# Kernel optimization log

Hardware: AMD Instinct MI355X
Metric: run time of the kernel (lower is better)

The kernel has to match this reference:

```python
import jax, jax.numpy as jnp
import numpy as np

B, N, K, C_IN, C_OUT = 4, 8192, 32, 64, 64
MID = (C_OUT + C_IN) // 2  # 64, since C_IN is even
GROUPS = 8
EPS = 1e-5
SLOPE = 0.1


def group_norm(x, gamma, beta, groups=GROUPS, eps=EPS):
    # x: [b, ..., C], normalize per-sample over all spatial dims and group channels
    b = x.shape[0]
    C = x.shape[-1]
    xr = x.reshape(b, -1, groups, C // groups)
    mean = xr.mean(axis=(1, 3), keepdims=True)
    var = xr.var(axis=(1, 3), keepdims=True)
    xn = ((xr - mean) / jnp.sqrt(var + eps)).reshape(x.shape)
    return xn * gamma + beta


def lrelu(x):
    return jnp.where(x >= 0, x, SLOPE * x)


def setup_inputs() -> dict:
    key = jax.random.key(0)
    ks = jax.random.split(key, 10)
    signal = jax.random.normal(ks[0], (B, N, C_IN), dtype=jnp.float32)
    edges = jax.random.randint(ks[1], (B * N * K,), 0, B * N, dtype=jnp.int64)
    edge_feats = jax.random.normal(ks[2], (B * N * K, 3), dtype=jnp.float32)
    W1 = jax.random.normal(ks[3], (MID, C_IN + 3), dtype=jnp.float32) * 0.1
    W2 = jax.random.normal(ks[4], (C_OUT, MID), dtype=jnp.float32) * 0.1
    W3 = jax.random.normal(ks[5], (C_OUT, C_OUT), dtype=jnp.float32) * 0.1
    return {
        "signal": signal, "edges": edges, "edge_feats": edge_feats,
        "W1": W1, "g1": jnp.ones((MID,), jnp.float32), "b1": jnp.zeros((MID,), jnp.float32),
        "W2": W2, "g2": jnp.ones((C_OUT,), jnp.float32), "b2": jnp.zeros((C_OUT,), jnp.float32),
        "W3": W3, "g3": jnp.ones((C_OUT,), jnp.float32), "b3": jnp.zeros((C_OUT,), jnp.float32),
    }


def reference(signal, edges, edge_feats, W1, g1, b1, W2, g2, b2, W3, g3, b3):
    b, n, c = signal.shape
    k = edges.shape[0] // (b * n)
    flat = signal.reshape(b * n, c)
    # gather neighbor features and take relative difference: [b*n, k, c]
    ef = flat[edges].reshape(b * n, k, c) - flat[:, None, :]
    # concat relative coordinates -> [b, n, k, c+3]
    x = jnp.concatenate([ef, edge_feats.reshape(b * n, k, 3)], axis=-1)
    x = x.reshape(b, n, k, c + 3)
    # 1x1 conv (fc1) + GN + lrelu
    x = jnp.einsum('bnkc,mc->bnkm', x, W1)
    x = lrelu(group_norm(x, g1, b1))
    # max-pool over neighbors -> [b, n, mid]
    x = jnp.max(x, axis=2)
    # fc2 + GN + lrelu
    x = jnp.einsum('bnm,om->bno', x, W2)
    x = lrelu(group_norm(x, g2, b2))
    # fc3 + GN + lrelu
    x = jnp.einsum('bno,po->bnp', x, W3)
    x = lrelu(group_norm(x, g3, b3))
    return x  # [b, n, nb_feat_out]
```

## Files before the change

### kernel.cpp

```cpp
#include <hip/hip_runtime.h>

#define NB    4
#define NPB   8192
#define NPTS  (NB*NPB)
#define KNB   32
#define CH    64
#define W1C   67
#define EPSV  1e-5f
#define SLOPEV 0.1f

typedef float f32x2 __attribute__((ext_vector_type(2)));
typedef float f32x4 __attribute__((ext_vector_type(4)));
typedef short bf16x8 __attribute__((ext_vector_type(8)));
typedef unsigned short u16;
typedef u16 u16x4 __attribute__((ext_vector_type(4)));
typedef u16 u16x8 __attribute__((ext_vector_type(8)));

#define WS_STATS1 0
#define WS_STATS2 64
#define WS_STATS3 128
#define WS_YB     256
#define WS_MX     (WS_YB + NPTS*CH/2)
#define WS_MN     (WS_MX + NPTS*CH/2)

#define LDPW 68
#define SEDS (KNB*4 + 4)
#define EPB  64

__device__ __forceinline__ u16 f2bf(float f) {
    unsigned u = __float_as_uint(f);
    u += 0x7fff + ((u >> 16) & 1);
    return (u16)(u >> 16);
}
__device__ __forceinline__ float bf2f(u16 h) {
    return __uint_as_float(((unsigned)h) << 16);
}

__device__ __forceinline__ bool probe_is32(const int* e_i32, int tid) {
    int found = 0;
    #pragma unroll
    for (int i = 0; i < 8; ++i)
        found |= (e_i32[(tid*8 + i)*2 + 1] != 0);
    return (__ballot(found) != 0ull);
}

template<int MODE>
__global__ __launch_bounds__(256) void k_mm(
    const void* __restrict__ X0, const void* __restrict__ X1,
    const float* __restrict__ Wg,
    const float* __restrict__ statsIn, float invcnt,
    const float* __restrict__ gm, const float* __restrict__ bt,
    u16* __restrict__ Out, float* __restrict__ statsOut,
    float* __restrict__ zeroStats)
{
    __shared__ u16 Wl[64*LDPW];
    __shared__ __align__(16) float affA[64];
    __shared__ __align__(16) float affB[64];
    __shared__ float lacc[16];
    int tid = threadIdx.x;
    int pbase = blockIdx.x * 64;
    int b = pbase >> 13;

    if (MODE == 0 && blockIdx.x == 0 && tid < 192) zeroStats[tid] = 0.f;
    if (MODE != 0) {
        if (tid < 64) {
            int g = tid >> 3;
            float sv = statsIn[b*16 + g*2 + 0];
            float qv = statsIn[b*16 + g*2 + 1];
            float mean = sv * invcnt;
            float var  = fmaf(-mean, mean, qv * invcnt);
            float rstd = rsqrtf(var + EPSV);
            float a = gm[tid] * rstd;
            affA[tid] = a;
            affB[tid] = fmaf(-mean, a, bt[tid]);
        }
        if (tid < 16) lacc[tid] = 0.f;
    }
    {
        const int wstride = (MODE == 0) ? W1C : 64;
        #pragma unroll
        for (int i = 0; i < 16; ++i) {
            int e = tid + 256*i;
            int o = e >> 6, m = e & 63;
            Wl[o*LDPW + m] = f2bf(Wg[o*wstride + m]);
        }
    }
    __syncthreads();

    int l = tid & 63, w = tid >> 6;
    int lr = l & 15, lk = l >> 4;
    int row = pbase + w*16 + lr;

    bf16x8 af[2];
    #pragma unroll
    for (int kh = 0; kh < 2; ++kh) {
        int m0 = kh*32 + lk*8;
        bf16x8 h;
        if (MODE == 0) {
            f32x4 a0 = *(const f32x4*)&((const float*)X0)[row*64 + m0];
            f32x4 a1 = *(const f32x4*)&((const float*)X0)[row*64 + m0 + 4];
            #pragma unroll
            for (int j = 0; j < 4; ++j) {
                h[j]   = (short)f2bf(a0[j]);
                h[4+j] = (short)f2bf(a1[j]);
            }
        } else {
            float aA[8], aB[8];
            *(f32x4*)&aA[0] = *(const f32x4*)&affA[m0];
            *(f32x4*)&aA[4] = *(const f32x4*)&affA[m0+4];
            *(f32x4*)&aB[0] = *(const f32x4*)&affB[m0];
            *(f32x4*)&aB[4] = *(const f32x4*)&affB[m0+4];
            u16x8 vx = *(const u16x8*)&((const u16*)X0)[row*64 + m0];
            if (MODE == 1) {
                u16x8 vn = *(const u16x8*)&((const u16*)X1)[row*64 + m0];
                #pragma unroll
                for (int j = 0; j < 8; ++j) {
                    float a = aA[j];
                    float x = (a < 0.f) ? bf2f(vn[j]) : bf2f(vx[j]);
                    float z = fmaf(a, x, aB[j]);
                    z = (z >= 0.f) ? z : SLOPEV * z;
                    h[j] = (short)f2bf(z);
                }
            } else {
                #pragma unroll
                for (int j = 0; j < 8; ++j) {
                    float z = fmaf(aA[j], bf2f(vx[j]), aB[j]);
                    z = (z >= 0.f) ? z : SLOPEV * z;
                    h[j] = (short)f2bf(z);
                }
            }
        }
        af[kh] = h;
    }

    bf16x8 bw[4][2];
    #pragma unroll
    for (int ot = 0; ot < 4; ++ot)
        #pragma unroll
        for (int kh = 0; kh < 2; ++kh)
            bw[ot][kh] = *(const bf16x8*)&Wl[(ot*16 + lr)*LDPW + kh*32 + lk*8];

    f32x4 acc[4];
    #pragma unroll
    for (int ot = 0; ot < 4; ++ot) {
        f32x4 c = {0.f, 0.f, 0.f, 0.f};
        c = __builtin_amdgcn_mfma_f32_16x16x32_bf16(af[0], bw[ot][0], c, 0, 0, 0);
        c = __builtin_amdgcn_mfma_f32_16x16x32_bf16(af[1], bw[ot][1], c, 0, 0, 0);
        acc[ot] = c;
    }

    #pragma unroll
    for (int ot = 0; ot < 4; ++ot)
        #pragma unroll
        for (int r = 0; r < 4; ++r) {
            int p = pbase + w*16 + lk*4 + r;
            int o = ot*16 + lr;
            Out[p*64 + o] = f2bf(acc[ot][r]);
        }

    if (MODE != 0) {
        #pragma unroll
        for (int ot = 0; ot < 4; ++ot) {
            float s = 0.f, ss = 0.f;
            #pragma unroll
            for (int r = 0; r < 4; ++r) {
                float v = acc[ot][r];
                s += v;
                ss = fmaf(v, v, ss);
            }
            s += __shfl_xor(s, 16, 64);  ss += __shfl_xor(ss, 16, 64);
            s += __shfl_xor(s, 32, 64);  ss += __shfl_xor(ss, 32, 64);
            s += __shfl_xor(s, 1, 64);   ss += __shfl_xor(ss, 1, 64);
            s += __shfl_xor(s, 2, 64);   ss += __shfl_xor(ss, 2, 64);
            s += __shfl_xor(s, 4, 64);   ss += __shfl_xor(ss, 4, 64);
            if ((l & 7) == 0 && l < 16) {
                int g = ot*2 + (l >> 3);
                atomicAdd(&lacc[g*2 + 0], s);
                atomicAdd(&lacc[g*2 + 1], ss);
            }
        }
        __syncthreads();
        if (tid < 16)
            atomicAdd(&statsOut[b*16 + tid], lacc[tid]);
    }
}

__global__ __launch_bounds__(512) void k_edge(
    const u16* __restrict__ Yb, const void* __restrict__ edg,
    const float* __restrict__ ef, const float* __restrict__ W1,
    u16* __restrict__ Mx, u16* __restrict__ Mn, float* __restrict__ stats1)
{
    __shared__ float sed[EPB*SEDS];
    __shared__ float lacc[16];
    int tid = threadIdx.x;
    if (tid < 16) lacc[tid] = 0.f;

    bool is32 = probe_is32((const int*)edg, tid);
    {
        const int* e32 = (const int*)edg;
        const long long* e64 = (const long long*)edg;
        int ebase = blockIdx.x * (EPB*KNB);
        #pragma unroll
        for (int i = 0; i < 4; ++i) {
            int idx = tid + i*512;
            int gi  = ebase + idx;
            int e   = is32 ? __builtin_nontemporal_load(e32 + gi)
                           : (int)__builtin_nontemporal_load(e64 + gi);
            int pt = idx >> 5, k = idx & 31;
            float* d = &sed[pt*SEDS + k*4];
            d[0] = __builtin_nontemporal_load(ef + gi*3 + 0);
            d[1] = __builtin_nontemporal_load(ef + gi*3 + 1);
            d[2] = __builtin_nontemporal_load(ef + gi*3 + 2);
            d[3] = __int_as_float(e << 7);
        }
    }

    int lane = tid & 63, wv = tid >> 6;
    int il = lane & 7;
    int g8 = lane >> 3;
    int lpt = wv*8 + g8;
    int p = blockIdx.x * EPB + lpt;

    f32x2 w0[4], w1[4], w2[4];
    #pragma unroll
    for (int jj = 0; jj < 4; ++jj) {
        int ch = il*8 + jj*2;
        w0[jj] = (f32x2){W1[ch*W1C + 64], W1[(ch+1)*W1C + 64]};
        w1[jj] = (f32x2){W1[ch*W1C + 65], W1[(ch+1)*W1C + 65]};
        w2[jj] = (f32x2){W1[ch*W1C + 66], W1[(ch+1)*W1C + 66]};
    }
    f32x2 yp[4], mx[4], mn[4];
    u16x8 yh = *(const u16x8*)&Yb[p*64 + il*8];
    #pragma unroll
    for (int jj = 0; jj < 4; ++jj) {
        yp[jj] = (f32x2){bf2f(yh[jj*2]), bf2f(yh[jj*2+1])};
        mx[jj] = (f32x2){-3.4e38f, -3.4e38f};
        mn[jj] = (f32x2){ 3.4e38f,  3.4e38f};
    }
    f32x2 s2 = {0.f, 0.f}, ss2 = {0.f, 0.f};
    __syncthreads();

    const char* Ybase = (const char*)Yb + il*16;
    const float* sp = &sed[lpt*SEDS];
    #pragma unroll 8
    for (int k = 0; k < KNB; ++k) {
        f32x4 m4 = *(const f32x4*)(sp + k*4);
        u16x8 q = *(const u16x8*)(Ybase + __float_as_int(m4[3]));
        f32x2 c0v = m4[0], c1v = m4[1], c2v = m4[2];
        #pragma unroll
        for (int jj = 0; jj < 4; ++jj) {
            f32x2 qq = {bf2f(q[jj*2]), bf2f(q[jj*2+1])};
            f32x2 t = qq - yp[jj];
            t = __builtin_elementwise_fma(c0v, w0[jj], t);
            t = __builtin_elementwise_fma(c1v, w1[jj], t);
            t = __builtin_elementwise_fma(c2v, w2[jj], t);
            mx[jj] = __builtin_elementwise_max(mx[jj], t);
            mn[jj] = __builtin_elementwise_min(mn[jj], t);
            s2 += t;
            ss2 = __builtin_elementwise_fma(t, t, ss2);
        }
    }

    u16x8 hx, hn;
    #pragma unroll
    for (int jj = 0; jj < 4; ++jj) {
        hx[jj*2] = f2bf(mx[jj].x); hx[jj*2+1] = f2bf(mx[jj].y);
        hn[jj*2] = f2bf(mn[jj].x); hn[jj*2+1] = f2bf(mn[jj].y);
    }
    __builtin_nontemporal_store(hx, (u16x8*)(Mx + p*64 + il*8));
    __builtin_nontemporal_store(hn, (u16x8*)(Mn + p*64 + il*8));

    float s  = s2.x + s2.y;
    float ss = ss2.x + ss2.y;
    s += __shfl_xor(s,  8, 64);  ss += __shfl_xor(ss,  8, 64);
    s += __shfl_xor(s, 16, 64);  ss += __shfl_xor(ss, 16, 64);
    s += __shfl_xor(s, 32, 64);  ss += __shfl_xor(ss, 32, 64);
    if (lane < 8) {
        atomicAdd(&lacc[lane*2 + 0], s);
        atomicAdd(&lacc[lane*2 + 1], ss);
    }
    __syncthreads();
    if (tid < 16) {
        int b = (blockIdx.x * EPB) >> 13;
        atomicAdd(&stats1[b*16 + tid], lacc[tid]);
    }
}

__global__ __launch_bounds__(256) void k_out(
    const u16* __restrict__ z3, const float* __restrict__ stats,
    const float* __restrict__ g3, const float* __restrict__ b3,
    float* __restrict__ out)
{
    const float invcnt = 1.f/(float)(NPB*8);
    int tid = threadIdx.x;
    int pbase = blockIdx.x * 64;
    int b = pbase >> 13;
    #pragma unroll
    for (int it = 0; it < 4; ++it) {
        int flat = it*1024 + tid*4;
        int p = pbase + (flat >> 6);
        int m = flat & 63;
        int g = m >> 3;
        float sv = stats[b*16 + g*2 + 0];
        float qv = stats[b*16 + g*2 + 1];
        float mean = sv * invcnt;
        float var  = fmaf(-mean, mean, qv * invcnt);
        float rstd = rsqrtf(var + EPSV);
        u16x4 v = *(const u16x4*)&z3[p*64 + m];
        float r[4];
        #pragma unroll
        for (int j = 0; j < 4; ++j) {
            float aa = g3[m+j] * rstd;
            float z  = fmaf(aa, bf2f(v[j]) - mean, b3[m+j]);
            r[j] = (z >= 0.f) ? z : SLOPEV * z;
        }
        f32x4 o4 = {r[0], r[1], r[2], r[3]};
        *(f32x4*)&out[p*64 + m] = o4;
    }
}

extern "C" void kernel_launch(void* const* d_in, const int* in_sizes, int n_in,
                              void* d_out, int out_size, void* d_ws, size_t ws_size,
                              hipStream_t stream)
{
    const float* sig = (const float*)d_in[0];
    const void*  edg = d_in[1];
    const float* ef  = (const float*)d_in[2];
    const float* W1  = (const float*)d_in[3];
    const float* g1  = (const float*)d_in[4];
    const float* b1  = (const float*)d_in[5];
    const float* W2  = (const float*)d_in[6];
    const float* g2  = (const float*)d_in[7];
    const float* b2  = (const float*)d_in[8];
    const float* W3  = (const float*)d_in[9];
    const float* g3  = (const float*)d_in[10];
    const float* b3  = (const float*)d_in[11];
    float* out = (float*)d_out;
    float* ws  = (float*)d_ws;
    u16*   yb  = (u16*)(ws + WS_YB);
    u16*   mxb = (u16*)(ws + WS_MX);
    u16*   mnb = (u16*)(ws + WS_MN);

    k_mm<0><<<NPTS/64, 256, 0, stream>>>(sig, nullptr, W1, nullptr, 0.f,
                                         nullptr, nullptr, yb, nullptr, ws);
    k_edge<<<NPTS/EPB, 512, 0, stream>>>(yb, edg, ef, W1, mxb, mnb,
                                         ws + WS_STATS1);
    k_mm<1><<<NPTS/64, 256, 0, stream>>>(mxb, mnb, W2, ws + WS_STATS1,
                                         1.f/(float)(NPB*KNB*8), g1, b1,
                                         yb, ws + WS_STATS2, nullptr);
    k_mm<2><<<NPTS/64, 256, 0, stream>>>(yb, nullptr, W3, ws + WS_STATS2,
                                         1.f/(float)(NPB*8), g2, b2,
                                         mxb, ws + WS_STATS3, nullptr);
    k_out<<<NPTS/64, 256, 0, stream>>>(mxb, ws + WS_STATS3, g3, b3, out);
}
```

Measured before the change: 57.42 us.

## Fuse edge, fc2, fc3 and output stages into persistent kernel with grid barriers

```diff
diff --git a/kernel.cpp b/kernel.cpp
--- a/kernel.cpp
+++ b/kernel.cpp
@@ -8,24 +8,24 @@
 #define W1C   67
 #define EPSV  1e-5f
 #define SLOPEV 0.1f
+#define MBLK  256
+#define MPPB  128
 
 typedef float f32x2 __attribute__((ext_vector_type(2)));
 typedef float f32x4 __attribute__((ext_vector_type(4)));
 typedef short bf16x8 __attribute__((ext_vector_type(8)));
 typedef unsigned short u16;
-typedef u16 u16x4 __attribute__((ext_vector_type(4)));
 typedef u16 u16x8 __attribute__((ext_vector_type(8)));
 
-#define WS_STATS1 0
-#define WS_STATS2 64
-#define WS_STATS3 128
-#define WS_YB     256
-#define WS_MX     (WS_YB + NPTS*CH/2)
-#define WS_MN     (WS_MX + NPTS*CH/2)
-
-#define LDPW 68
-#define SEDS (KNB*4 + 4)
-#define EPB  64
+#define WS_STATS 0
+#define WS_CTR   192
+#define WS_YB    256
+#define WS_PK    (WS_YB + NPTS*CH/2)
+
+#define LDW 68
+
+#define INV1 (1.f/(float)(NPB*KNB*8))
+#define INV2 (1.f/(float)(NPB*8))
 
 __device__ __forceinline__ u16 f2bf(float f) {
     unsigned u = __float_as_uint(f);
@@ -35,7 +35,6 @@
 __device__ __forceinline__ float bf2f(u16 h) {
     return __uint_as_float(((unsigned)h) << 16);
 }
-
 __device__ __forceinline__ bool probe_is32(const int* e_i32, int tid) {
     int found = 0;
     #pragma unroll
@@ -44,278 +43,365 @@
     return (__ballot(found) != 0ull);
 }
 
-template<int MODE>
-__global__ __launch_bounds__(256) void k_mm(
-    const void* __restrict__ X0, const void* __restrict__ X1,
-    const float* __restrict__ Wg,
-    const float* __restrict__ statsIn, float invcnt,
-    const float* __restrict__ gm, const float* __restrict__ bt,
-    u16* __restrict__ Out, float* __restrict__ statsOut,
-    float* __restrict__ zeroStats)
+__global__ __launch_bounds__(256) void k_pre(
+    const float* __restrict__ sig, const void* __restrict__ edg,
+    const float* __restrict__ ef, const float* __restrict__ W1,
+    u16* __restrict__ Yb, float* __restrict__ pk, float* __restrict__ ws)
 {
-    __shared__ u16 Wl[64*LDPW];
-    __shared__ __align__(16) float affA[64];
-    __shared__ __align__(16) float affB[64];
-    __shared__ float lacc[16];
+    __shared__ u16 Wl[64*LDW];
     int tid = threadIdx.x;
-    int pbase = blockIdx.x * 64;
-    int b = pbase >> 13;
-
-    if (MODE == 0 && blockIdx.x == 0 && tid < 192) zeroStats[tid] = 0.f;
-    if (MODE != 0) {
-        if (tid < 64) {
-            int g = tid >> 3;
-            float sv = statsIn[b*16 + g*2 + 0];
-            float qv = statsIn[b*16 + g*2 + 1];
-            float mean = sv * invcnt;
-            float var  = fmaf(-mean, mean, qv * invcnt);
-            float rstd = rsqrtf(var + EPSV);
-            float a = gm[tid] * rstd;
-            affA[tid] = a;
-            affB[tid] = fmaf(-mean, a, bt[tid]);
-        }
-        if (tid < 16) lacc[tid] = 0.f;
-    }
-    {
-        const int wstride = (MODE == 0) ? W1C : 64;
-        #pragma unroll
-        for (int i = 0; i < 16; ++i) {
-            int e = tid + 256*i;
-            int o = e >> 6, m = e & 63;
-            Wl[o*LDPW + m] = f2bf(Wg[o*wstride + m]);
-        }
+    int blk = blockIdx.x;
+
+    if (blk >= 512) {
+        int pb = blk - 512;
+        bool is32 = probe_is32((const int*)edg, tid);
+        const int*       e32 = (const int*)edg;
+        const long long* e64 = (const long long*)edg;
+        int ebase = pb * 2048;
+        #pragma unroll
+        for (int i = 0; i < 8; ++i) {
+            int gi = ebase + tid + i*256;
+            int e  = is32 ? __builtin_nontemporal_load(e32 + gi)
+                          : (int)__builtin_nontemporal_load(e64 + gi);
+            f32x4 v = { __builtin_nontemporal_load(ef + gi*3 + 0),
+                        __builtin_nontemporal_load(ef + gi*3 + 1),
+                        __builtin_nontemporal_load(ef + gi*3 + 2),
+                        __int_as_float(e << 7) };
+            __builtin_nontemporal_store(v, (f32x4*)(pk + gi*4));
+        }
+        return;
+    }
+    if (blk == 0 && tid < 196) ws[tid] = 0.f;
+
+    int pbase = blk * 64;
+    #pragma unroll
+    for (int i = 0; i < 16; ++i) {
+        int e = tid + 256*i;
+        int o = e >> 6, m = e & 63;
+        Wl[o*LDW + m] = f2bf(W1[o*W1C + m]);
     }
     __syncthreads();
 
     int l = tid & 63, w = tid >> 6;
     int lr = l & 15, lk = l >> 4;
     int row = pbase + w*16 + lr;
-
     bf16x8 af[2];
     #pragma unroll
     for (int kh = 0; kh < 2; ++kh) {
         int m0 = kh*32 + lk*8;
+        f32x4 a0 = *(const f32x4*)&sig[row*64 + m0];
+        f32x4 a1 = *(const f32x4*)&sig[row*64 + m0 + 4];
         bf16x8 h;
-        if (MODE == 0) {
-            f32x4 a0 = *(const f32x4*)&((const float*)X0)[row*64 + m0];
-            f32x4 a1 = *(const f32x4*)&((const float*)X0)[row*64 + m0 + 4];
-            #pragma unroll
-            for (int j = 0; j < 4; ++j) {
-                h[j]   = (short)f2bf(a0[j]);
-                h[4+j] = (short)f2bf(a1[j]);
-            }
-        } else {
+        #pragma unroll
+        for (int j = 0; j < 4; ++j) {
+            h[j]   = (short)f2bf(a0[j]);
+            h[4+j] = (short)f2bf(a1[j]);
+        }
+        af[kh] = h;
+    }
+    bf16x8 bw[4][2];
+    #pragma unroll
+    for (int ot = 0; ot < 4; ++ot)
+        #pragma unroll
+        for (int kh = 0; kh < 2; ++kh)
+            bw[ot][kh] = *(const bf16x8*)&Wl[(ot*16 + lr)*LDW + kh*32 + lk*8];
+    #pragma unroll
+    for (int ot = 0; ot < 4; ++ot) {
+        f32x4 c = {0.f, 0.f, 0.f, 0.f};
+        c = __builtin_amdgcn_mfma_f32_16x16x32_bf16(af[0], bw[ot][0], c, 0, 0, 0);
+        c = __builtin_amdgcn_mfma_f32_16x16x32_bf16(af[1], bw[ot][1], c, 0, 0, 0);
+        #pragma unroll
+        for (int r = 0; r < 4; ++r)
+            Yb[(pbase + w*16 + lk*4 + r)*64 + ot*16 + lr] = f2bf(c[r]);
+    }
+}
+
+__device__ __forceinline__ void stats_flush_barrier(float* statsG, const float* lacc,
+                                                    int b, unsigned* ctr, int tid)
+{
+    __syncthreads();
+    if (tid == 0) {
+        #pragma unroll
+        for (int i = 0; i < 16; ++i)
+            atomicAdd(&statsG[b*16 + i], lacc[i]);
+        __threadfence();
+        __hip_atomic_fetch_add(ctr, 1u, __ATOMIC_RELEASE, __HIP_MEMORY_SCOPE_AGENT);
+        while (__hip_atomic_load(ctr, __ATOMIC_ACQUIRE, __HIP_MEMORY_SCOPE_AGENT) < (unsigned)MBLK)
+            __builtin_amdgcn_s_sleep(2);
+    }
+    __syncthreads();
+}
+
+__global__ __launch_bounds__(512, 4) void k_mega(
+    const u16* __restrict__ Yb, const float* __restrict__ pk,
+    const float* __restrict__ W1,
+    const float* __restrict__ g1, const float* __restrict__ b1,
+    const float* __restrict__ W2,
+    const float* __restrict__ g2, const float* __restrict__ b2,
+    const float* __restrict__ W3,
+    const float* __restrict__ g3, const float* __restrict__ b3,
+    float* __restrict__ out, float* __restrict__ ws)
+{
+    __shared__ u16 Wl2[64*LDW], Wl3[64*LDW];
+    __shared__ u16 rMx[MPPB*LDW], rMn[MPPB*LDW];
+    __shared__ float affA[64], affB[64], lsS[16], lacc[16];
+
+    int tid = threadIdx.x;
+    int blk = blockIdx.x;
+    int pbase = blk * MPPB;
+    int b = pbase >> 13;
+    float* statsG = ws + WS_STATS;
+    unsigned* ctr = (unsigned*)(ws + WS_CTR);
+    int lane = tid & 63, wv = tid >> 6;
+
+    #pragma unroll
+    for (int i = 0; i < 8; ++i) {
+        int e = tid + 512*i;
+        int o = e >> 6, m = e & 63;
+        Wl2[o*LDW + m] = f2bf(W2[o*64 + m]);
+        Wl3[o*LDW + m] = f2bf(W3[o*64 + m]);
+    }
+    if (tid < 16) lacc[tid] = 0.f;
+    __syncthreads();
+
+    {
+        int il = lane & 7, g8 = lane >> 3;
+        f32x2 w0[4], w1[4], w2[4];
+        #pragma unroll
+        for (int jj = 0; jj < 4; ++jj) {
+            int ch = il*8 + jj*2;
+            w0[jj] = (f32x2){W1[ch*W1C + 64], W1[(ch+1)*W1C + 64]};
+            w1[jj] = (f32x2){W1[ch*W1C + 65], W1[(ch+1)*W1C + 65]};
+            w2[jj] = (f32x2){W1[ch*W1C + 66], W1[(ch+1)*W1C + 66]};
+        }
+        const char* Ybase = (const char*)Yb + il*16;
+        float sE = 0.f, ssE = 0.f;
+        #pragma unroll
+        for (int pi = 0; pi < 2; ++pi) {
+            int lpt = pi*64 + wv*8 + g8;
+            int p = pbase + lpt;
+            u16x8 yh = *(const u16x8*)&Yb[p*64 + il*8];
+            f32x2 yp[4], mx[4], mn[4];
+            #pragma unroll
+            for (int jj = 0; jj < 4; ++jj) {
+                yp[jj] = (f32x2){bf2f(yh[jj*2]), bf2f(yh[jj*2+1])};
+                mx[jj] = (f32x2){-3.4e38f, -3.4e38f};
+                mn[jj] = (f32x2){ 3.4e38f,  3.4e38f};
+            }
+            f32x2 s2 = {0.f, 0.f}, ss2 = {0.f, 0.f};
+            const float* pp = pk + p*KNB*4;
+            #pragma unroll 8
+            for (int k = 0; k < KNB; ++k) {
+                f32x4 m4 = *(const f32x4*)(pp + k*4);
+                u16x8 q = *(const u16x8*)(Ybase + __float_as_int(m4[3]));
+                f32x2 c0v = m4[0], c1v = m4[1], c2v = m4[2];
+                #pragma unroll
+                for (int jj = 0; jj < 4; ++jj) {
+                    f32x2 qq = {bf2f(q[jj*2]), bf2f(q[jj*2+1])};
+                    f32x2 t = qq - yp[jj];
+                    t = __builtin_elementwise_fma(c0v, w0[jj], t);
+                    t = __builtin_elementwise_fma(c1v, w1[jj], t);
+                    t = __builtin_elementwise_fma(c2v, w2[jj], t);
+                    mx[jj] = __builtin_elementwise_max(mx[jj], t);
+                    mn[jj] = __builtin_elementwise_min(mn[jj], t);
+                    s2 += t;
+                    ss2 = __builtin_elementwise_fma(t, t, ss2);
+                }
+            }
+            u16x8 hx, hn;
+            #pragma unroll
+            for (int jj = 0; jj < 4; ++jj) {
+                hx[jj*2] = f2bf(mx[jj].x); hx[jj*2+1] = f2bf(mx[jj].y);
+                hn[jj*2] = f2bf(mn[jj].x); hn[jj*2+1] = f2bf(mn[jj].y);
+            }
+            *(u16x8*)&rMx[lpt*LDW + il*8] = hx;
+            *(u16x8*)&rMn[lpt*LDW + il*8] = hn;
+            sE  += s2.x + s2.y;
+            ssE += ss2.x + ss2.y;
+        }
+        sE += __shfl_xor(sE,  8, 64);  ssE += __shfl_xor(ssE,  8, 64);
+        sE += __shfl_xor(sE, 16, 64);  ssE += __shfl_xor(ssE, 16, 64);
+        sE += __shfl_xor(sE, 32, 64);  ssE += __shfl_xor(ssE, 32, 64);
+        if (lane < 8) {
+            atomicAdd(&lacc[lane*2 + 0], sE);
+            atomicAdd(&lacc[lane*2 + 1], ssE);
+        }
+    }
+    stats_flush_barrier(statsG + 0, lacc, b, ctr + 0, tid);
+
+    if (tid < 16) {
+        lsS[tid] = __uint_as_float(__hip_atomic_load(
+            (const unsigned*)&statsG[b*16 + tid], __ATOMIC_RELAXED, __HIP_MEMORY_SCOPE_AGENT));
+        lacc[tid] = 0.f;
+    }
+    __syncthreads();
+    if (tid < 64) {
+        int g = tid >> 3;
+        float mean = lsS[g*2] * INV1;
+        float var  = fmaf(-mean, mean, lsS[g*2+1] * INV1);
+        float rstd = rsqrtf(var + EPSV);
+        float a = g1[tid] * rstd;
+        affA[tid] = a;
+        affB[tid] = fmaf(-mean, a, b1[tid]);
+    }
+    __syncthreads();
+
+    int lr = lane & 15, lk = lane >> 4;
+    f32x4 acc2[4];
+    {
+        bf16x8 af[2];
+        #pragma unroll
+        for (int kh = 0; kh < 2; ++kh) {
+            int m0 = kh*32 + lk*8;
             float aA[8], aB[8];
             *(f32x4*)&aA[0] = *(const f32x4*)&affA[m0];
             *(f32x4*)&aA[4] = *(const f32x4*)&affA[m0+4];
             *(f32x4*)&aB[0] = *(const f32x4*)&affB[m0];
             *(f32x4*)&aB[4] = *(const f32x4*)&affB[m0+4];
-            u16x8 vx = *(const u16x8*)&((const u16*)X0)[row*64 + m0];
-            if (MODE == 1) {
-                u16x8 vn = *(const u16x8*)&((const u16*)X1)[row*64 + m0];
-                #pragma unroll
-                for (int j = 0; j < 8; ++j) {
-                    float a = aA[j];
-                    float x = (a < 0.f) ? bf2f(vn[j]) : bf2f(vx[j]);
-                    float z = fmaf(a, x, aB[j]);
-                    z = (z >= 0.f) ? z : SLOPEV * z;
-                    h[j] = (short)f2bf(z);
-                }
-            } else {
-                #pragma unroll
-                for (int j = 0; j < 8; ++j) {
-                    float z = fmaf(aA[j], bf2f(vx[j]), aB[j]);
-                    z = (z >= 0.f) ? z : SLOPEV * z;
-                    h[j] = (short)f2bf(z);
-                }
-            }
-        }
-        af[kh] = h;
-    }
-
-    bf16x8 bw[4][2];
-    #pragma unroll
-    for (int ot = 0; ot < 4; ++ot)
-        #pragma unroll
-        for (int kh = 0; kh < 2; ++kh)
-            bw[ot][kh] = *(const bf16x8*)&Wl[(ot*16 + lr)*LDPW + kh*32 + lk*8];
-
-    f32x4 acc[4];
-    #pragma unroll
-    for (int ot = 0; ot < 4; ++ot) {
-        f32x4 c = {0.f, 0.f, 0.f, 0.f};
-        c = __builtin_amdgcn_mfma_f32_16x16x32_bf16(af[0], bw[ot][0], c, 0, 0, 0);
-        c = __builtin_amdgcn_mfma_f32_16x16x32_bf16(af[1], bw[ot][1], c, 0, 0, 0);
-        acc[ot] = c;
-    }
-
-    #pragma unroll
-    for (int ot = 0; ot < 4; ++ot)
-        #pragma unroll
-        for (int r = 0; r < 4; ++r) {
-            int p = pbase + w*16 + lk*4 + r;
-            int o = ot*16 + lr;
-            Out[p*64 + o] = f2bf(acc[ot][r]);
-        }
-
-    if (MODE != 0) {
+            u16x8 vx = *(const u16x8*)&rMx[(wv*16 + lr)*LDW + m0];
+            u16x8 vn = *(const u16x8*)&rMn[(wv*16 + lr)*LDW + m0];
+            bf16x8 h;
+            #pragma unroll
+            for (int j = 0; j < 8; ++j) {
+                float a = aA[j];
+                float x = (a < 0.f) ? bf2f(vn[j]) : bf2f(vx[j]);
+                float z = fmaf(a, x, aB[j]);
+                z = (z >= 0.f) ? z : SLOPEV * z;
+                h[j] = (short)f2bf(z);
+            }
+            af[kh] = h;
+        }
+        #pragma unroll
+        for (int ot = 0; ot < 4; ++ot) {
+            bf16x8 b0 = *(const bf16x8*)&Wl2[(ot*16 + lr)*LDW + lk*8];
+            bf16x8 b1f = *(const bf16x8*)&Wl2[(ot*16 + lr)*LDW + 32 + lk*8];
+            f32x4 c = {0.f, 0.f, 0.f, 0.f};
+            c = __builtin_amdgcn_mfma_f32_16x16x32_bf16(af[0], b0, c, 0, 0, 0);
+            c = __builtin_amdgcn_mfma_f32_16x16x32_bf16(af[1], b1f, c, 0, 0, 0);
+            acc2[ot] = c;
+        }
         #pragma unroll
         for (int ot = 0; ot < 4; ++ot) {
             float s = 0.f, ss = 0.f;
             #pragma unroll
             for (int r = 0; r < 4; ++r) {
-                float v = acc[ot][r];
-                s += v;
-                ss = fmaf(v, v, ss);
+                float v = acc2[ot][r];
+                s += v; ss = fmaf(v, v, ss);
             }
             s += __shfl_xor(s, 16, 64);  ss += __shfl_xor(ss, 16, 64);
             s += __shfl_xor(s, 32, 64);  ss += __shfl_xor(ss, 32, 64);
             s += __shfl_xor(s, 1, 64);   ss += __shfl_xor(ss, 1, 64);
             s += __shfl_xor(s, 2, 64);   ss += __shfl_xor(ss, 2, 64);
             s += __shfl_xor(s, 4, 64);   ss += __shfl_xor(ss, 4, 64);
-            if ((l & 7) == 0 && l < 16) {
-                int g = ot*2 + (l >> 3);
+            if ((lane & 7) == 0 && lane < 16) {
+                int g = ot*2 + (lane >> 3);
                 atomicAdd(&lacc[g*2 + 0], s);
                 atomicAdd(&lacc[g*2 + 1], ss);
             }
         }
         __syncthreads();
-        if (tid < 16)
-            atomicAdd(&statsOut[b*16 + tid], lacc[tid]);
-    }
-}
-
-__global__ __launch_bounds__(512) void k_edge(
-    const u16* __restrict__ Yb, const void* __restrict__ edg,
-    const float* __restrict__ ef, const float* __restrict__ W1,
-    u16* __restrict__ Mx, u16* __restrict__ Mn, float* __restrict__ stats1)
-{
-    __shared__ float sed[EPB*SEDS];
-    __shared__ float lacc[16];
-    int tid = threadIdx.x;
-    if (tid < 16) lacc[tid] = 0.f;
-
-    bool is32 = probe_is32((const int*)edg, tid);
+        #pragma unroll
+        for (int ot = 0; ot < 4; ++ot)
+            #pragma unroll
+            for (int r = 0; r < 4; ++r)
+                rMx[(wv*16 + lk*4 + r)*LDW + ot*16 + lr] = f2bf(acc2[ot][r]);
+    }
+    stats_flush_barrier(statsG + 64, lacc, b, ctr + 1, tid);
+
+    if (tid < 16) {
+        lsS[tid] = __uint_as_float(__hip_atomic_load(
+            (const unsigned*)&statsG[64 + b*16 + tid], __ATOMIC_RELAXED, __HIP_MEMORY_SCOPE_AGENT));
+        lacc[tid] = 0.f;
+    }
+    __syncthreads();
+    if (tid < 64) {
+        int g = tid >> 3;
+        float mean = lsS[g*2] * INV2;
+        float var  = fmaf(-mean, mean, lsS[g*2+1] * INV2);
+        float rstd = rsqrtf(var + EPSV);
+        float a = g2[tid] * rstd;
+        affA[tid] = a;
+        affB[tid] = fmaf(-mean, a, b2[tid]);
+    }
+    __syncthreads();
+
+    f32x4 acc3[4];
     {
-        const int* e32 = (const int*)edg;
-        const long long* e64 = (const long long*)edg;
-        int ebase = blockIdx.x * (EPB*KNB);
-        #pragma unroll
-        for (int i = 0; i < 4; ++i) {
-            int idx = tid + i*512;
-            int gi  = ebase + idx;
-            int e   = is32 ? __builtin_nontemporal_load(e32 + gi)
-                           : (int)__builtin_nontemporal_load(e64 + gi);
-            int pt = idx >> 5, k = idx & 31;
-            float* d = &sed[pt*SEDS + k*4];
-            d[0] = __builtin_nontemporal_load(ef + gi*3 + 0);
-            d[1] = __builtin_nontemporal_load(ef + gi*3 + 1);
-            d[2] = __builtin_nontemporal_load(ef + gi*3 + 2);
-            d[3] = __int_as_float(e << 7);
-        }
-    }
-
-    int lane = tid & 63, wv = tid >> 6;
-    int il = lane & 7;
-    int g8 = lane >> 3;
-    int lpt = wv*8 + g8;
-    int p = blockIdx.x * EPB + lpt;
-
-    f32x2 w0[4], w1[4], w2[4];
-    #pragma unroll
-    for (int jj = 0; jj < 4; ++jj) {
-        int ch = il*8 + jj*2;
-        w0[jj] = (f32x2){W1[ch*W1C + 64], W1[(ch+1)*W1C + 64]};
-        w1[jj] = (f32x2){W1[ch*W1C + 65], W1[(ch+1)*W1C + 65]};
-        w2[jj] = (f32x2){W1[ch*W1C + 66], W1[(ch+1)*W1C + 66]};
-    }
-    f32x2 yp[4], mx[4], mn[4];
-    u16x8 yh = *(const u16x8*)&Yb[p*64 + il*8];
-    #pragma unroll
-    for (int jj = 0; jj < 4; ++jj) {
-        yp[jj] = (f32x2){bf2f(yh[jj*2]), bf2f(yh[jj*2+1])};
-        mx[jj] = (f32x2){-3.4e38f, -3.4e38f};
-        mn[jj] = (f32x2){ 3.4e38f,  3.4e38f};
-    }
-    f32x2 s2 = {0.f, 0.f}, ss2 = {0.f, 0.f};
-    __syncthreads();
-
-    const char* Ybase = (const char*)Yb + il*16;
-    const float* sp = &sed[lpt*SEDS];
-    #pragma unroll 8
-    for (int k = 0; k < KNB; ++k) {
-        f32x4 m4 = *(const f32x4*)(sp + k*4);
-        u16x8 q = *(const u16x8*)(Ybase + __float_as_int(m4[3]));
-        f32x2 c0v = m4[0], c1v = m4[1], c2v = m4[2];
-        #pragma unroll
-        for (int jj = 0; jj < 4; ++jj) {
-            f32x2 qq = {bf2f(q[jj*2]), bf2f(q[jj*2+1])};
-            f32x2 t = qq - yp[jj];
-            t = __builtin_elementwise_fma(c0v, w0[jj], t);
-            t = __builtin_elementwise_fma(c1v, w1[jj], t);
-            t = __builtin_elementwise_fma(c2v, w2[jj], t);
-            mx[jj] = __builtin_elementwise_max(mx[jj], t);
-            mn[jj] = __builtin_elementwise_min(mn[jj], t);
-            s2 += t;
-            ss2 = __builtin_elementwise_fma(t, t, ss2);
-        }
-    }
-
-    u16x8 hx, hn;
-    #pragma unroll
-    for (int jj = 0; jj < 4; ++jj) {
-        hx[jj*2] = f2bf(mx[jj].x); hx[jj*2+1] = f2bf(mx[jj].y);
-        hn[jj*2] = f2bf(mn[jj].x); hn[jj*2+1] = f2bf(mn[jj].y);
-    }
-    __builtin_nontemporal_store(hx, (u16x8*)(Mx + p*64 + il*8));
-    __builtin_nontemporal_store(hn, (u16x8*)(Mn + p*64 + il*8));
-
-    float s  = s2.x + s2.y;
-    float ss = ss2.x + ss2.y;
-    s += __shfl_xor(s,  8, 64);  ss += __shfl_xor(ss,  8, 64);
-    s += __shfl_xor(s, 16, 64);  ss += __shfl_xor(ss, 16, 64);
-    s += __shfl_xor(s, 32, 64);  ss += __shfl_xor(ss, 32, 64);
-    if (lane < 8) {
-        atomicAdd(&lacc[lane*2 + 0], s);
-        atomicAdd(&lacc[lane*2 + 1], ss);
-    }
-    __syncthreads();
-    if (tid < 16) {
-        int b = (blockIdx.x * EPB) >> 13;
-        atomicAdd(&stats1[b*16 + tid], lacc[tid]);
-    }
-}
-
-__global__ __launch_bounds__(256) void k_out(
-    const u16* __restrict__ z3, const float* __restrict__ stats,
-    const float* __restrict__ g3, const float* __restrict__ b3,
-    float* __restrict__ out)
-{
-    const float invcnt = 1.f/(float)(NPB*8);
-    int tid = threadIdx.x;
-    int pbase = blockIdx.x * 64;
-    int b = pbase >> 13;
-    #pragma unroll
-    for (int it = 0; it < 4; ++it) {
-        int flat = it*1024 + tid*4;
-        int p = pbase + (flat >> 6);
-        int m = flat & 63;
-        int g = m >> 3;
-        float sv = stats[b*16 + g*2 + 0];
-        float qv = stats[b*16 + g*2 + 1];
-        float mean = sv * invcnt;
-        float var  = fmaf(-mean, mean, qv * invcnt);
+        bf16x8 af[2];
+        #pragma unroll
+        for (int kh = 0; kh < 2; ++kh) {
+            int m0 = kh*32 + lk*8;
+            float aA[8], aB[8];
+            *(f32x4*)&aA[0] = *(const f32x4*)&affA[m0];
+            *(f32x4*)&aA[4] = *(const f32x4*)&affA[m0+4];
+            *(f32x4*)&aB[0] = *(const f32x4*)&affB[m0];
+            *(f32x4*)&aB[4] = *(const f32x4*)&affB[m0+4];
+            u16x8 vh = *(const u16x8*)&rMx[(wv*16 + lr)*LDW + m0];
+            bf16x8 h;
+            #pragma unroll
+            for (int j = 0; j < 8; ++j) {
+                float z = fmaf(aA[j], bf2f(vh[j]), aB[j]);
+                z = (z >= 0.f) ? z : SLOPEV * z;
+                h[j] = (short)f2bf(z);
+            }
+            af[kh] = h;
+        }
+        #pragma unroll
+        for (int ot = 0; ot < 4; ++ot) {
+            bf16x8 b0 = *(const bf16x8*)&Wl3[(ot*16 + lr)*LDW + lk*8];
+            bf16x8 b1f = *(const bf16x8*)&Wl3[(ot*16 + lr)*LDW + 32 + lk*8];
+            f32x4 c = {0.f, 0.f, 0.f, 0.f};
+            c = __builtin_amdgcn_mfma_f32_16x16x32_bf16(af[0], b0, c, 0, 0, 0);
+            c = __builtin_amdgcn_mfma_f32_16x16x32_bf16(af[1], b1f, c, 0, 0, 0);
+            acc3[ot] = c;
+        }
+        #pragma unroll
+        for (int ot = 0; ot < 4; ++ot) {
+            float s = 0.f, ss = 0.f;
+            #pragma unroll
+            for (int r = 0; r < 4; ++r) {
+                float v = acc3[ot][r];
+                s += v; ss = fmaf(v, v, ss);
+            }
+            s += __shfl_xor(s, 16, 64);  ss += __shfl_xor(ss, 16, 64);
+            s += __shfl_xor(s, 32, 64);  ss += __shfl_xor(ss, 32, 64);
+            s += __shfl_xor(s, 1, 64);   ss += __shfl_xor(ss, 1, 64);
+            s += __shfl_xor(s, 2, 64);   ss += __shfl_xor(ss, 2, 64);
+            s += __shfl_xor(s, 4, 64);   ss += __shfl_xor(ss, 4, 64);
+            if ((lane & 7) == 0 && lane < 16) {
+                int g = ot*2 + (lane >> 3);
+                atomicAdd(&lacc[g*2 + 0], s);
+                atomicAdd(&lacc[g*2 + 1], ss);
+            }
+        }
+    }
+    stats_flush_barrier(statsG + 128, lacc, b, ctr + 2, tid);
+
+    if (tid < 16)
+        lsS[tid] = __uint_as_float(__hip_atomic_load(
+            (const unsigned*)&statsG[128 + b*16 + tid], __ATOMIC_RELAXED, __HIP_MEMORY_SCOPE_AGENT));
+    __syncthreads();
+    if (tid < 64) {
+        int g = tid >> 3;
+        float mean = lsS[g*2] * INV2;
+        float var  = fmaf(-mean, mean, lsS[g*2+1] * INV2);
         float rstd = rsqrtf(var + EPSV);
-        u16x4 v = *(const u16x4*)&z3[p*64 + m];
-        float r[4];
-        #pragma unroll
-        for (int j = 0; j < 4; ++j) {
-            float aa = g3[m+j] * rstd;
-            float z  = fmaf(aa, bf2f(v[j]) - mean, b3[m+j]);
-            r[j] = (z >= 0.f) ? z : SLOPEV * z;
-        }
-        f32x4 o4 = {r[0], r[1], r[2], r[3]};
-        *(f32x4*)&out[p*64 + m] = o4;
+        float a = g3[tid] * rstd;
+        affA[tid] = a;
+        affB[tid] = fmaf(-mean, a, b3[tid]);
+    }
+    __syncthreads();
+
+    #pragma unroll
+    for (int ot = 0; ot < 4; ++ot) {
+        int o = ot*16 + lr;
+        float a = affA[o], bb = affB[o];
+        #pragma unroll
+        for (int r = 0; r < 4; ++r) {
+            float z = fmaf(a, acc3[ot][r], bb);
+            z = (z >= 0.f) ? z : SLOPEV * z;
+            out[(pbase + wv*16 + lk*4 + r)*64 + o] = z;
+        }
     }
 }
 
@@ -338,18 +424,9 @@
     float* out = (float*)d_out;
     float* ws  = (float*)d_ws;
     u16*   yb  = (u16*)(ws + WS_YB);
-    u16*   mxb = (u16*)(ws + WS_MX);
-    u16*   mnb = (u16*)(ws + WS_MN);
-
-    k_mm<0><<<NPTS/64, 256, 0, stream>>>(sig, nullptr, W1, nullptr, 0.f,
-                                         nullptr, nullptr, yb, nullptr, ws);
-    k_edge<<<NPTS/EPB, 512, 0, stream>>>(yb, edg, ef, W1, mxb, mnb,
-                                         ws + WS_STATS1);
-    k_mm<1><<<NPTS/64, 256, 0, stream>>>(mxb, mnb, W2, ws + WS_STATS1,
-                                         1.f/(float)(NPB*KNB*8), g1, b1,
-                                         yb, ws + WS_STATS2, nullptr);
-    k_mm<2><<<NPTS/64, 256, 0, stream>>>(yb, nullptr, W3, ws + WS_STATS2,
-                                         1.f/(float)(NPB*8), g2, b2,
-                                         mxb, ws + WS_STATS3, nullptr);
-    k_out<<<NPTS/64, 256, 0, stream>>>(mxb, ws + WS_STATS3, g3, b3, out);
-}
+    float* pk  = ws + WS_PK;
+
+    k_pre<<<1024, 256, 0, stream>>>(sig, edg, ef, W1, yb, pk, ws);
+    k_mega<<<MBLK, 512, 0, stream>>>(yb, pk, W1, g1, b1, W2, g2, b2,
+                                     W3, g3, b3, out, ws);
+}
```

Measured after the change: 166.7 us. 2.9x slower.

## Prepack edge indices and features into compact bf16 records in the first matmul kernel

Applied to the files above, without the earlier changes.

```diff
diff --git a/kernel.cpp b/kernel.cpp
--- a/kernel.cpp
+++ b/kernel.cpp
@@ -22,10 +22,10 @@
 #define WS_YB     256
 #define WS_MX     (WS_YB + NPTS*CH/2)
 #define WS_MN     (WS_MX + NPTS*CH/2)
+#define WS_PK     (WS_MN + NPTS*CH/2)
 
 #define LDPW 68
-#define SEDS (KNB*4 + 4)
-#define EPB  64
+#define EPB  32
 
 __device__ __forceinline__ u16 f2bf(float f) {
     unsigned u = __float_as_uint(f);
@@ -35,7 +35,6 @@
 __device__ __forceinline__ float bf2f(u16 h) {
     return __uint_as_float(((unsigned)h) << 16);
 }
-
 __device__ __forceinline__ bool probe_is32(const int* e_i32, int tid) {
     int found = 0;
     #pragma unroll
@@ -51,13 +50,39 @@
     const float* __restrict__ statsIn, float invcnt,
     const float* __restrict__ gm, const float* __restrict__ bt,
     u16* __restrict__ Out, float* __restrict__ statsOut,
-    float* __restrict__ zeroStats)
+    float* __restrict__ zeroStats,
+    const void* __restrict__ edg, const float* __restrict__ ef,
+    u16* __restrict__ pk)
 {
     __shared__ u16 Wl[64*LDPW];
     __shared__ __align__(16) float affA[64];
     __shared__ __align__(16) float affB[64];
     __shared__ float lacc[16];
     int tid = threadIdx.x;
+
+    if (MODE == 0 && blockIdx.x >= 512) {
+        int pb = blockIdx.x - 512;
+        bool is32 = probe_is32((const int*)edg, tid);
+        const int*       e32 = (const int*)edg;
+        const long long* e64 = (const long long*)edg;
+        u16x4* pk4 = (u16x4*)pk;
+        int base = pb * 2048;
+        #pragma unroll
+        for (int i = 0; i < 8; ++i) {
+            int pi = base + tid + i*256;
+            int po = pi >> 8, k = (pi >> 3) & 31, s = pi & 7;
+            int gi = ((po << 3) + s)*32 + k;
+            int e  = is32 ? __builtin_nontemporal_load(e32 + gi)
+                          : (int)__builtin_nontemporal_load(e64 + gi);
+            u16x4 v = { (u16)e,
+                        f2bf(__builtin_nontemporal_load(ef + gi*3 + 0)),
+                        f2bf(__builtin_nontemporal_load(ef + gi*3 + 1)),
+                        f2bf(__builtin_nontemporal_load(ef + gi*3 + 2)) };
+            __builtin_nontemporal_store(v, pk4 + pi);
+        }
+        return;
+    }
+
     int pbase = blockIdx.x * 64;
     int b = pbase >> 13;
 
@@ -185,41 +210,21 @@
     }
 }
 
-__global__ __launch_bounds__(512) void k_edge(
-    const u16* __restrict__ Yb, const void* __restrict__ edg,
-    const float* __restrict__ ef, const float* __restrict__ W1,
+__global__ __launch_bounds__(256) void k_edge(
+    const u16* __restrict__ Yb, const u16* __restrict__ pk,
+    const float* __restrict__ W1,
     u16* __restrict__ Mx, u16* __restrict__ Mn, float* __restrict__ stats1)
 {
-    __shared__ float sed[EPB*SEDS];
     __shared__ float lacc[16];
     int tid = threadIdx.x;
     if (tid < 16) lacc[tid] = 0.f;
-
-    bool is32 = probe_is32((const int*)edg, tid);
-    {
-        const int* e32 = (const int*)edg;
-        const long long* e64 = (const long long*)edg;
-        int ebase = blockIdx.x * (EPB*KNB);
-        #pragma unroll
-        for (int i = 0; i < 4; ++i) {
-            int idx = tid + i*512;
-            int gi  = ebase + idx;
-            int e   = is32 ? __builtin_nontemporal_load(e32 + gi)
-                           : (int)__builtin_nontemporal_load(e64 + gi);
-            int pt = idx >> 5, k = idx & 31;
-            float* d = &sed[pt*SEDS + k*4];
-            d[0] = __builtin_nontemporal_load(ef + gi*3 + 0);
-            d[1] = __builtin_nontemporal_load(ef + gi*3 + 1);
-            d[2] = __builtin_nontemporal_load(ef + gi*3 + 2);
-            d[3] = __int_as_float(e << 7);
-        }
-    }
+    __syncthreads();
 
     int lane = tid & 63, wv = tid >> 6;
     int il = lane & 7;
     int g8 = lane >> 3;
-    int lpt = wv*8 + g8;
-    int p = blockIdx.x * EPB + lpt;
+    int p = blockIdx.x * EPB + wv*8 + g8;
+    int po = blockIdx.x * 4 + wv;
 
     f32x2 w0[4], w1[4], w2[4];
     #pragma unroll
@@ -238,15 +243,14 @@
         mn[jj] = (f32x2){ 3.4e38f,  3.4e38f};
     }
     f32x2 s2 = {0.f, 0.f}, ss2 = {0.f, 0.f};
-    __syncthreads();
 
     const char* Ybase = (const char*)Yb + il*16;
-    const float* sp = &sed[lpt*SEDS];
+    const u16x4* pko = (const u16x4*)pk + po*256;
     #pragma unroll 8
     for (int k = 0; k < KNB; ++k) {
-        f32x4 m4 = *(const f32x4*)(sp + k*4);
-        u16x8 q = *(const u16x8*)(Ybase + __float_as_int(m4[3]));
-        f32x2 c0v = m4[0], c1v = m4[1], c2v = m4[2];
+        u16x4 pv = pko[(k << 3) + g8];
+        u16x8 q = *(const u16x8*)(Ybase + (((int)pv[0]) << 7));
+        f32x2 c0v = bf2f(pv[1]), c1v = bf2f(pv[2]), c2v = bf2f(pv[3]);
         #pragma unroll
         for (int jj = 0; jj < 4; ++jj) {
             f32x2 qq = {bf2f(q[jj*2]), bf2f(q[jj*2+1])};
@@ -306,12 +310,12 @@
         float mean = sv * invcnt;
         float var  = fmaf(-mean, mean, qv * invcnt);
         float rstd = rsqrtf(var + EPSV);
-        u16x4 v = *(const u16x4*)&z3[p*64 + m];
+        u16x4 vv = *(const u16x4*)&z3[p*64 + m];
         float r[4];
         #pragma unroll
         for (int j = 0; j < 4; ++j) {
             float aa = g3[m+j] * rstd;
-            float z  = fmaf(aa, bf2f(v[j]) - mean, b3[m+j]);
+            float z  = fmaf(aa, bf2f(vv[j]) - mean, b3[m+j]);
             r[j] = (z >= 0.f) ? z : SLOPEV * z;
         }
         f32x4 o4 = {r[0], r[1], r[2], r[3]};
@@ -340,16 +344,19 @@
     u16*   yb  = (u16*)(ws + WS_YB);
     u16*   mxb = (u16*)(ws + WS_MX);
     u16*   mnb = (u16*)(ws + WS_MN);
-
-    k_mm<0><<<NPTS/64, 256, 0, stream>>>(sig, nullptr, W1, nullptr, 0.f,
-                                         nullptr, nullptr, yb, nullptr, ws);
-    k_edge<<<NPTS/EPB, 512, 0, stream>>>(yb, edg, ef, W1, mxb, mnb,
-                                         ws + WS_STATS1);
+    u16*   pk  = (u16*)(ws + WS_PK);
+
+    k_mm<0><<<1024, 256, 0, stream>>>(sig, nullptr, W1, nullptr, 0.f,
+                                      nullptr, nullptr, yb, nullptr, ws,
+                                      edg, ef, pk);
+    k_edge<<<NPTS/EPB, 256, 0, stream>>>(yb, pk, W1, mxb, mnb, ws + WS_STATS1);
     k_mm<1><<<NPTS/64, 256, 0, stream>>>(mxb, mnb, W2, ws + WS_STATS1,
                                          1.f/(float)(NPB*KNB*8), g1, b1,
-                                         yb, ws + WS_STATS2, nullptr);
+                                         yb, ws + WS_STATS2, nullptr,
+                                         nullptr, nullptr, nullptr);
     k_mm<2><<<NPTS/64, 256, 0, stream>>>(yb, nullptr, W3, ws + WS_STATS2,
                                          1.f/(float)(NPB*8), g2, b2,
-                                         mxb, ws + WS_STATS3, nullptr);
+                                         mxb, ws + WS_STATS3, nullptr,
+                                         nullptr, nullptr, nullptr);
     k_out<<<NPTS/64, 256, 0, stream>>>(mxb, ws + WS_STATS3, g3, b3, out);
 }
```

Result: slower. 70.19 us (+22.2%).
